# Kernel tuning notes

Hardware: AMD Instinct MI355X
Metric: run time of the kernel (lower is better)

The kernel has to match this reference:

```python
import jax, jax.numpy as jnp
import numpy as np

B, S, D, H, EXPAND = 4, 2048, 256, 4, 4
DH = D // H
EPS = 1e-3  # keras BatchNormalization default epsilon
NEG = -1e9  # keras Softmax masking constant


def setup_inputs() -> dict:
    key = jax.random.key(0)
    ks = jax.random.split(key, 8)
    x = jax.random.normal(ks[0], (B, S, D), dtype=jnp.float32)
    mask = jax.random.randint(ks[1], (B, S), 0, 2) > 0
    mask = mask.at[:, 0].set(True)  # ensure each row has a valid token
    sc = 1.0 / np.sqrt(D)
    return {
        "x": x,
        "mask": mask,
        "bn1_gamma": jnp.ones((D,), jnp.float32),
        "bn1_beta": jnp.zeros((D,), jnp.float32),
        "bn1_mean": jax.random.normal(ks[2], (D,), jnp.float32) * 0.1,
        "bn1_var": jnp.ones((D,), jnp.float32),
        "qkv_w": jax.random.normal(ks[3], (D, 3 * D), jnp.float32) * sc,
        "proj_w": jax.random.normal(ks[4], (D, D), jnp.float32) * sc,
        "bn2_gamma": jnp.ones((D,), jnp.float32),
        "bn2_beta": jnp.zeros((D,), jnp.float32),
        "bn2_mean": jax.random.normal(ks[5], (D,), jnp.float32) * 0.1,
        "bn2_var": jnp.ones((D,), jnp.float32),
        "w1": jax.random.normal(ks[6], (D, EXPAND * D), jnp.float32) * sc,
        "w2": jax.random.normal(ks[7], (EXPAND * D, D), jnp.float32) * (sc / 2.0),
    }


def _bn(x, gamma, beta, mean, var):
    # inference-mode BatchNormalization over the channel axis
    return (x - mean) * jax.lax.rsqrt(var + EPS) * gamma + beta


def reference(x, mask, bn1_gamma, bn1_beta, bn1_mean, bn1_var, qkv_w, proj_w,
              bn2_gamma, bn2_beta, bn2_mean, bn2_var, w1, w2):
    scale = D ** (-0.5)
    # --- attention sub-block ---
    skip = x
    h = _bn(x, bn1_gamma, bn1_beta, bn1_mean, bn1_var)
    qkv = h @ qkv_w                                    # [B,S,3D]
    qkv = qkv.reshape(B, S, H, 3 * DH).transpose(0, 2, 1, 3)  # [B,H,S,3dh]
    q, k, v = qkv[..., :DH], qkv[..., DH:2 * DH], qkv[..., 2 * DH:]
    scores = jnp.einsum('bhqd,bhkd->bhqk', q, k) * scale      # [B,H,S,S]
    scores = scores + jnp.where(mask[:, None, None, :], 0.0, NEG)
    attn = jax.nn.softmax(scores, axis=-1)
    o = jnp.einsum('bhqk,bhkd->bhqd', attn, v)                # [B,H,S,dh]
    o = o.transpose(0, 2, 1, 3).reshape(B, S, D) @ proj_w
    x = o + skip
    # --- FFN sub-block ---
    skip = x
    h = _bn(x, bn2_gamma, bn2_beta, bn2_mean, bn2_var)
    h = jax.nn.swish(h @ w1)                                  # [B,S,4D]
    h = h @ w2
    return h + skip
```

## Files before the change

kernel.cpp:

```cpp
#include <hip/hip_runtime.h>
#include <math.h>

#define S_ 2048
#define D_ 256
#define B_ 4
#define H_ 4

typedef __attribute__((ext_vector_type(8))) short  bh8;
typedef __attribute__((ext_vector_type(4))) float  fx4;
typedef __attribute__((ext_vector_type(4))) unsigned short us4;
typedef __attribute__((ext_vector_type(4))) unsigned int   ux4;

__device__ inline unsigned short bf16r(float f) {
    unsigned int u = __builtin_bit_cast(unsigned int, f);
    return (unsigned short)((u + 0x7FFFu + ((u >> 16) & 1u)) >> 16);
}
__device__ inline unsigned int cvtpk(float a, float b) {
    unsigned int r;
    asm("v_cvt_pk_bf16_f32 %0, %1, %2" : "=v"(r) : "v"(a), "v"(b));
    return r;
}
__device__ inline float vexp2(float x) {
    float r;
    asm volatile("v_exp_f32 %0, %1\n\ts_nop 1" : "=v"(r) : "v"(x));
    return r;
}
__device__ inline void gl_lds16(const unsigned short* g, unsigned short* l) {
    __builtin_amdgcn_global_load_lds(
        (const __attribute__((address_space(1))) unsigned int*)g,
        (__attribute__((address_space(3))) unsigned int*)l, 16, 0, 0);
}
#define DRAIN_BARRIER() asm volatile("s_waitcnt vmcnt(0)\n\ts_barrier" ::: "memory")

__device__ inline size_t fragoff(int m, int k, int K32) {
    return ((size_t)(m >> 4) * K32 + (k >> 5)) * 512
         + (size_t)((((k >> 3) & 3) * 16 + (m & 15)) * 8 + (k & 7));
}

__global__ __launch_bounds__(256) void prep_all_k(
    const float* __restrict__ qkv_w, const float* __restrict__ proj_w,
    const float* __restrict__ w1,    const float* __restrict__ w2,
    unsigned short* __restrict__ qkv_wt, unsigned short* __restrict__ proj_wf,
    unsigned short* __restrict__ w1f,    unsigned short* __restrict__ w2f,
    const float* __restrict__ x,
    const float* __restrict__ g1, const float* __restrict__ b1,
    const float* __restrict__ m1, const float* __restrict__ v1,
    unsigned short* __restrict__ xb,
    const int* __restrict__ mask, float* __restrict__ maskf)
{
    const int bidx = blockIdx.x;
    if (bidx < 768) {
        const float* W; unsigned short* Wt; int K, N, u0; bool frag;
        if (bidx < 192)      { W = qkv_w;  Wt = qkv_wt; K = 256;  N = 768;  u0 = bidx * 256;        frag = false; }
        else if (bidx < 256) { W = proj_w; Wt = proj_wf; K = 256;  N = 256;  u0 = (bidx - 192) * 256; frag = true; }
        else if (bidx < 512) { W = w1;     Wt = w1f;    K = 256;  N = 1024; u0 = (bidx - 256) * 256; frag = true; }
        else                 { W = w2;     Wt = w2f;    K = 1024; N = 256;  u0 = (bidx - 512) * 256; frag = true; }
        const int u = u0 + threadIdx.x;
        const int k4 = u / N, n = u % N;
        us4 tv;
        #pragma unroll
        for (int j = 0; j < 4; ++j) tv[j] = bf16r(W[(size_t)(k4 * 4 + j) * N + n]);
        if (frag) *(us4*)&Wt[fragoff(n, k4 * 4, K >> 5)] = tv;
        else      *(us4*)&Wt[(size_t)n * K + k4 * 4] = tv;
    } else if (bidx < 2816) {
        const int i = (bidx - 768) * 256 + threadIdx.x;
        const int c4 = (i & 63) * 4;
        float4 xv = *(const float4*)&x[(size_t)i * 4];
        float vv[4] = {xv.x, xv.y, xv.z, xv.w};
        us4 tv;
        #pragma unroll
        for (int j = 0; j < 4; ++j) {
            int c = c4 + j;
            float s = g1[c] * rsqrtf(v1[c] + 1e-3f);
            tv[j] = bf16r(vv[j] * s + (b1[c] - m1[c] * s));
        }
        *(us4*)&xb[(size_t)i * 4] = tv;
    } else {
        const int i = (bidx - 2816) * 256 + threadIdx.x;
        maskf[i] = mask[i] ? 0.0f : -1e9f;
    }
}

__global__ __launch_bounds__(256) void gemm_qkv_k(
    const unsigned short* __restrict__ A, const unsigned short* __restrict__ Wt,
    unsigned short* __restrict__ qf_o, unsigned short* __restrict__ kf_o,
    unsigned short* __restrict__ vf_o)
{
    constexpr int BM = 64, MI = 2, LA = 2;
    const int N = 768, K = 256;
    __shared__ unsigned short Asb[2][BM * 64];
    __shared__ unsigned short Bsb[2][128 * 64];

    const int n0 = blockIdx.x * 128, m0 = blockIdx.y * BM;
    const int t = threadIdx.x, w = t >> 6, l = t & 63;
    const int qi = l & 15, g = l >> 4;
    const int wm = w >> 1, wn = w & 1;
    const int lr = l >> 3, lc = (l & 7) * 8;
    (void)N;

    fx4 acc[MI][4];
    #pragma unroll
    for (int mi = 0; mi < MI; ++mi)
        #pragma unroll
        for (int ni = 0; ni < 4; ++ni) acc[mi][ni] = (fx4){0.f, 0.f, 0.f, 0.f};

    const int NT = K / 64;

#define STAGE(P, KT) {                                                        \
    const int kb = (KT) * 64;                                                 \
    _Pragma("unroll")                                                         \
    for (int i = 0; i < LA; ++i) {                                            \
        int r0 = (w * LA + i) * 8;                                            \
        gl_lds16(A + (size_t)(m0 + r0 + lr) * K + kb + lc, &Asb[P][r0 * 64]); \
    }                                                                         \
    _Pragma("unroll")                                                         \
    for (int i = 0; i < 4; ++i) {                                             \
        int r0 = (w * 4 + i) * 8;                                             \
        gl_lds16(Wt + (size_t)(n0 + r0 + lr) * K + kb + lc, &Bsb[P][r0 * 64]);\
    } }

    STAGE(0, 0);
    DRAIN_BARRIER();
    int p = 0;
    for (int kt = 0; kt < NT; ++kt) {
        if (kt + 1 < NT) STAGE(p ^ 1, kt + 1);
        #pragma unroll
        for (int kk = 0; kk < 2; ++kk) {
            bh8 af[MI], bf[4];
            #pragma unroll
            for (int mi = 0; mi < MI; ++mi)
                af[mi] = *(const bh8*)&Asb[p][(wm * (BM / 2) + mi * 16 + qi) * 64
                                             + kk * 32 + g * 8];
            #pragma unroll
            for (int ni = 0; ni < 4; ++ni)
                bf[ni] = *(const bh8*)&Bsb[p][(wn * 64 + ni * 16 + qi) * 64
                                             + kk * 32 + g * 8];
            #pragma unroll
            for (int mi = 0; mi < MI; ++mi)
                #pragma unroll
                for (int ni = 0; ni < 4; ++ni)
                    acc[mi][ni] = __builtin_amdgcn_mfma_f32_16x16x32_bf16(
                        af[mi], bf[ni], acc[mi][ni], 0, 0, 0);
        }
        DRAIN_BARRIER();
        p ^= 1;
    }
#undef STAGE

    const int mbase = m0 + wm * (BM / 2);
    #pragma unroll
    for (int ni = 0; ni < 4; ++ni) {
        const int nf = n0 + wn * 64 + ni * 16;
        const int h = nf / 192, rem = nf % 192;
        const int region = rem / 64;
        const int c = rem % 64 + qi;
        #pragma unroll
        for (int mi = 0; mi < MI; ++mi) {
            #pragma unroll
            for (int r = 0; r < 4; ++r) {
                const int m = mbase + mi * 16 + g * 4 + r;
                const int s = m & 2047;
                const size_t bh = (size_t)((m >> 11) * 4 + h);
                float a = acc[mi][ni][r];
                if (region < 2) {
                    size_t off = (((bh * 128 + (s >> 4)) * 2 + (c >> 5)) * 64
                                  + ((c >> 3) & 3) * 16 + (s & 15)) * 8 + (c & 7);
                    if (region == 0)
                        qf_o[off] = bf16r(a * (0.0625f * 1.44269504f));
                    else
                        kf_o[off] = bf16r(a);
                } else {
                    size_t off = ((((bh * 32 + (s >> 6)) * 4 + (c >> 4)) * 2
                                  + ((s >> 5) & 1)) * 64
                                  + ((s >> 3) & 3) * 16 + (c & 15)) * 8 + (s & 7);
                    vf_o[off] = bf16r(a);
                }
            }
        }
    }
}

__global__ __launch_bounds__(512) void fused_mlp_k(
    const unsigned short* __restrict__ ob,
    const unsigned short* __restrict__ proj_wf,
    const unsigned short* __restrict__ w1f,
    const unsigned short* __restrict__ w2f,
    const float* __restrict__ x,
    const float* __restrict__ g2, const float* __restrict__ b2,
    const float* __restrict__ m2, const float* __restrict__ v2,
    float* __restrict__ out)
{
    __shared__ unsigned short x2nb[8 * 512];
    __shared__ unsigned short h2[32 * 512];

    const int t = threadIdx.x, w = t >> 6, l = t & 63;
    const int qi = l & 15, g = l >> 4;
    const int mt = blockIdx.x;
    const int m0 = mt * 16;

    fx4 acc1[2];
    acc1[0] = (fx4){0.f, 0.f, 0.f, 0.f};
    acc1[1] = (fx4){0.f, 0.f, 0.f, 0.f};
    {
        const unsigned short* Ab = ob + (size_t)mt * 8 * 512 + l * 8;
        const unsigned short* B0 = proj_wf + ((size_t)(w * 2 + 0) * 8) * 512 + l * 8;
        const unsigned short* B1 = proj_wf + ((size_t)(w * 2 + 1) * 8) * 512 + l * 8;
        #pragma unroll
        for (int kt = 0; kt < 8; ++kt) {
            bh8 a  = *(const bh8*)(Ab + (size_t)kt * 512);
            bh8 b0 = *(const bh8*)(B0 + (size_t)kt * 512);
            bh8 b1 = *(const bh8*)(B1 + (size_t)kt * 512);
            acc1[0] = __builtin_amdgcn_mfma_f32_16x16x32_bf16(a, b0, acc1[0], 0, 0, 0);
            acc1[1] = __builtin_amdgcn_mfma_f32_16x16x32_bf16(a, b1, acc1[1], 0, 0, 0);
        }
    }
    float x2res[2][4];
    #pragma unroll
    for (int nt = 0; nt < 2; ++nt) {
        const int n = w * 32 + nt * 16 + qi;
        const float s2 = g2[n] * rsqrtf(v2[n] + 1e-3f);
        const float o2 = b2[n] - m2[n] * s2;
        #pragma unroll
        for (int r = 0; r < 4; ++r) {
            const int m = m0 + g * 4 + r;
            float rv = acc1[nt][r] + x[(size_t)m * 256 + n];
            x2res[nt][r] = rv;
            x2nb[w * 512 + ((nt * 2 + (qi >> 3)) * 16 + g * 4 + r) * 8 + (qi & 7)]
                = bf16r(rv * s2 + o2);
        }
    }
    __syncthreads();

    fx4 acc2[8];
    #pragma unroll
    for (int nt = 0; nt < 8; ++nt) acc2[nt] = (fx4){0.f, 0.f, 0.f, 0.f};
    {
        #pragma unroll
        for (int kt = 0; kt < 8; ++kt) {
            bh8 a = *(const bh8*)&x2nb[kt * 512 + l * 8];
            #pragma unroll
            for (int nt = 0; nt < 8; ++nt) {
                bh8 b = *(const bh8*)(w1f + ((size_t)(w * 8 + nt) * 8 + kt) * 512 + l * 8);
                acc2[nt] = __builtin_amdgcn_mfma_f32_16x16x32_bf16(a, b, acc2[nt], 0, 0, 0);
            }
        }
    }
    __syncthreads();
    #pragma unroll
    for (int nt = 0; nt < 8; ++nt) {
        #pragma unroll
        for (int r = 0; r < 4; ++r) {
            const int n = w * 128 + nt * 16 + qi;
            float a = acc2[nt][r];
            float hv = a / (1.0f + __expf(-a));
            h2[(n >> 5) * 512 + (((n >> 3) & 3) * 16 + g * 4 + r) * 8 + (n & 7)]
                = bf16r(hv);
        }
    }
    __syncthreads();

    fx4 acc3[2];
    acc3[0] = (fx4){0.f, 0.f, 0.f, 0.f};
    acc3[1] = (fx4){0.f, 0.f, 0.f, 0.f};
    {
        const unsigned short* B0 = w2f + ((size_t)(w * 2 + 0) * 32) * 512 + l * 8;
        const unsigned short* B1 = w2f + ((size_t)(w * 2 + 1) * 32) * 512 + l * 8;
        #pragma unroll 4
        for (int kt = 0; kt < 32; ++kt) {
            bh8 a  = *(const bh8*)&h2[kt * 512 + l * 8];
            bh8 b0 = *(const bh8*)(B0 + (size_t)kt * 512);
            bh8 b1 = *(const bh8*)(B1 + (size_t)kt * 512);
            acc3[0] = __builtin_amdgcn_mfma_f32_16x16x32_bf16(a, b0, acc3[0], 0, 0, 0);
            acc3[1] = __builtin_amdgcn_mfma_f32_16x16x32_bf16(a, b1, acc3[1], 0, 0, 0);
        }
    }
    #pragma unroll
    for (int nt = 0; nt < 2; ++nt) {
        #pragma unroll
        for (int r = 0; r < 4; ++r) {
            const int m = m0 + g * 4 + r;
            const int n = w * 32 + nt * 16 + qi;
            out[(size_t)m * 256 + n] = acc3[nt][r] + x2res[nt][r];
        }
    }
}

__global__ __launch_bounds__(256) void attn_mfma_k(
    const unsigned short* __restrict__ qf,
    const unsigned short* __restrict__ kf,
    const unsigned short* __restrict__ vf,
    const float* __restrict__ maskf,
    unsigned short* __restrict__ ob)
{
    __shared__ fx4  Ol[2][64][8];
    __shared__ float Ll[2][64][2];

    const int bid = blockIdx.x;
    const int bh = bid & 15, qt = bid >> 4;
    const int b = bh >> 2, h = bh & 3;
    const int t = threadIdx.x;
    const int w = t >> 6, lane = t & 63;
    const int g = lane >> 4, qi = lane & 15;
    const int qh = w & 1;
    const int khalf = w >> 1;

    bh8 qA0, qA1, qB0, qB1;
    {
        const unsigned short* qp =
            qf + (size_t)(bh * 128 + qt * 4 + qh * 2) * 1024 + lane * 8;
        qA0 = *(const bh8*)(qp);
        qA1 = *(const bh8*)(qp + 512);
        qB0 = *(const bh8*)(qp + 1024);
        qB1 = *(const bh8*)(qp + 1536);
    }

    fx4 oA[4], oB[4];
    #pragma unroll
    for (int dt = 0; dt < 4; ++dt) {
        oA[dt] = (fx4){0.f, 0.f, 0.f, 0.f};
        oB[dt] = (fx4){0.f, 0.f, 0.f, 0.f};
    }
    float lsA = 0.f, lsB = 0.f;

    const unsigned short* kcur = kf + (size_t)bh * 131072 + khalf * 65536 + lane * 8;
    const unsigned short* vcur = vf + (size_t)bh * 131072 + khalf * 65536 + lane * 8;
    const float* mcur = maskf + b * 2048 + khalf * 1024 + g * 4;

    bh8 kfA[4][2], kfB[4][2], afA[4][2], afB[4][2];
    fx4 mvA[4], mvB[4];

#define LOADK(KF, MV) {                                                       \
    KF[0][0] = *(const bh8*)(kcur);        KF[0][1] = *(const bh8*)(kcur + 512);  \
    KF[1][0] = *(const bh8*)(kcur + 1024); KF[1][1] = *(const bh8*)(kcur + 1536); \
    KF[2][0] = *(const bh8*)(kcur + 2048); KF[2][1] = *(const bh8*)(kcur + 2560); \
    KF[3][0] = *(const bh8*)(kcur + 3072); KF[3][1] = *(const bh8*)(kcur + 3584); \
    MV[0] = *(const fx4*)(mcur);      MV[1] = *(const fx4*)(mcur + 16);       \
    MV[2] = *(const fx4*)(mcur + 32); MV[3] = *(const fx4*)(mcur + 48);       \
    kcur += 4096; mcur += 64; }

#define LOADV(AF) {                                                           \
    AF[0][0] = *(const bh8*)(vcur);        AF[0][1] = *(const bh8*)(vcur + 512);  \
    AF[1][0] = *(const bh8*)(vcur + 1024); AF[1][1] = *(const bh8*)(vcur + 1536); \
    AF[2][0] = *(const bh8*)(vcur + 2048); AF[2][1] = *(const bh8*)(vcur + 2560); \
    AF[3][0] = *(const bh8*)(vcur + 3072); AF[3][1] = *(const bh8*)(vcur + 3584); \
    vcur += 4096; }

#define PROCESS(KF, AF, MV) {                                                 \
    fx4 sA[4], sB[4];                                                         \
    _Pragma("unroll")                                                         \
    for (int kt = 0; kt < 4; ++kt) {                                          \
        fx4 zA = MV[kt];                                                      \
        zA = __builtin_amdgcn_mfma_f32_16x16x32_bf16(KF[kt][0], qA0, zA, 0, 0, 0); \
        zA = __builtin_amdgcn_mfma_f32_16x16x32_bf16(KF[kt][1], qA1, zA, 0, 0, 0); \
        sA[kt] = zA;                                                          \
        fx4 zB = MV[kt];                                                      \
        zB = __builtin_amdgcn_mfma_f32_16x16x32_bf16(KF[kt][0], qB0, zB, 0, 0, 0); \
        zB = __builtin_amdgcn_mfma_f32_16x16x32_bf16(KF[kt][1], qB1, zB, 0, 0, 0); \
        sB[kt] = zB;                                                          \
    }                                                                         \
    unsigned int pkA[4][2], pkB[4][2];                                        \
    _Pragma("unroll")                                                         \
    for (int kt = 0; kt < 4; ++kt) {                                          \
        float a0 = vexp2(sA[kt][0]);                                          \
        float a1 = vexp2(sA[kt][1]);                                          \
        float a2 = vexp2(sA[kt][2]);                                          \
        float a3 = vexp2(sA[kt][3]);                                          \
        lsA += (a0 + a1) + (a2 + a3);                                         \
        pkA[kt][0] = cvtpk(a0, a1);                                           \
        pkA[kt][1] = cvtpk(a2, a3);                                           \
        float b0 = vexp2(sB[kt][0]);                                          \
        float b1 = vexp2(sB[kt][1]);                                          \
        float b2 = vexp2(sB[kt][2]);                                          \
        float b3 = vexp2(sB[kt][3]);                                          \
        lsB += (b0 + b1) + (b2 + b3);                                         \
        pkB[kt][0] = cvtpk(b0, b1);                                           \
        pkB[kt][1] = cvtpk(b2, b3);                                           \
    }                                                                         \
    _Pragma("unroll")                                                         \
    for (int c = 0; c < 2; ++c) {                                             \
        unsigned int bwA[4], bwB[4];                                          \
        _Pragma("unroll")                                                     \
        for (int wd = 0; wd < 4; ++wd) {                                      \
            int src = (2 * (g & 1) + (wd >> 1)) * 16 + qi;                    \
            unsigned int vaA = (unsigned int)__shfl((int)pkA[2 * c][wd & 1], src, 64);     \
            unsigned int vbA = (unsigned int)__shfl((int)pkA[2 * c + 1][wd & 1], src, 64); \
            bwA[wd] = (g >= 2) ? vbA : vaA;                                   \
            unsigned int vaB = (unsigned int)__shfl((int)pkB[2 * c][wd & 1], src, 64);     \
            unsigned int vbB = (unsigned int)__shfl((int)pkB[2 * c + 1][wd & 1], src, 64); \
            bwB[wd] = (g >= 2) ? vbB : vaB;                                   \
        }                                                                     \
        bh8 bfA = __builtin_bit_cast(bh8, (ux4){bwA[0], bwA[1], bwA[2], bwA[3]}); \
        bh8 bfB = __builtin_bit_cast(bh8, (ux4){bwB[0], bwB[1], bwB[2], bwB[3]}); \
        _Pragma("unroll")                                                     \
        for (int dt = 0; dt < 4; ++dt) {                                      \
            oA[dt] = __builtin_amdgcn_mfma_f32_16x16x32_bf16(AF[dt][c], bfA, oA[dt], 0, 0, 0); \
            oB[dt] = __builtin_amdgcn_mfma_f32_16x16x32_bf16(AF[dt][c], bfB, oB[dt], 0, 0, 0); \
        }                                                                     \
    } }

    LOADK(kfA, mvA);
    LOADV(afA);
    for (int it = 0; it < 16; it += 2) {
        LOADK(kfB, mvB);
        LOADV(afB);
        PROCESS(kfA, afA, mvA);
        if (it + 2 < 16) {
            LOADK(kfA, mvA);
            LOADV(afA);
        }
        PROCESS(kfB, afB, mvB);
    }
#undef LOADK
#undef LOADV
#undef PROCESS

    const int slot = w & 1;
    if (w >= 2) {
        #pragma unroll
        for (int dt = 0; dt < 4; ++dt) {
            Ol[slot][lane][dt]     = oA[dt];
            Ol[slot][lane][4 + dt] = oB[dt];
        }
        Ll[slot][lane][0] = lsA;
        Ll[slot][lane][1] = lsB;
    }
    __syncthreads();
    if (w < 2) {
        lsA += Ll[slot][lane][0];
        lsB += Ll[slot][lane][1];
        #pragma unroll
        for (int dt = 0; dt < 4; ++dt) {
            fx4 pa = Ol[slot][lane][dt], pb = Ol[slot][lane][4 + dt];
            oA[dt][0] += pa[0]; oA[dt][1] += pa[1]; oA[dt][2] += pa[2]; oA[dt][3] += pa[3];
            oB[dt][0] += pb[0]; oB[dt][1] += pb[1]; oB[dt][2] += pb[2]; oB[dt][3] += pb[3];
        }
        lsA += __shfl_xor(lsA, 16, 64);
        lsA += __shfl_xor(lsA, 32, 64);
        lsB += __shfl_xor(lsB, 16, 64);
        lsB += __shfl_xor(lsB, 32, 64);
        float invA = 1.0f / lsA, invB = 1.0f / lsB;
        const int mA = b * 2048 + qt * 64 + qh * 32 + qi;
        #pragma unroll
        for (int dt = 0; dt < 4; ++dt) {
            us4 ta, tb;
            #pragma unroll
            for (int r = 0; r < 4; ++r) {
                ta[r] = bf16r(oA[dt][r] * invA);
                tb[r] = bf16r(oB[dt][r] * invB);
            }
            const int n0 = h * 64 + dt * 16 + g * 4;
            *(us4*)&ob[fragoff(mA,      n0, 8)] = ta;
            *(us4*)&ob[fragoff(mA + 16, n0, 8)] = tb;
        }
    }
}

extern "C" void kernel_launch(void* const* d_in, const int* in_sizes, int n_in,
                              void* d_out, int out_size, void* d_ws, size_t ws_size,
                              hipStream_t stream) {
    const float* x      = (const float*)d_in[0];
    const int*   mask   = (const int*)  d_in[1];
    const float* bn1_g  = (const float*)d_in[2];
    const float* bn1_b  = (const float*)d_in[3];
    const float* bn1_m  = (const float*)d_in[4];
    const float* bn1_v  = (const float*)d_in[5];
    const float* qkv_w  = (const float*)d_in[6];
    const float* proj_w = (const float*)d_in[7];
    const float* bn2_g  = (const float*)d_in[8];
    const float* bn2_b  = (const float*)d_in[9];
    const float* bn2_m  = (const float*)d_in[10];
    const float* bn2_v  = (const float*)d_in[11];
    const float* w1     = (const float*)d_in[12];
    const float* w2     = (const float*)d_in[13];
    float* out = (float*)d_out;

    char* w8 = (char*)d_ws;
    unsigned short* qkv_wt  = (unsigned short*)(w8 + 0);
    unsigned short* proj_wf = (unsigned short*)(w8 + 393216);
    unsigned short* w1f     = (unsigned short*)(w8 + 524288);
    unsigned short* w2f     = (unsigned short*)(w8 + 1048576);
    float*          maskf   = (float*)         (w8 + 1572864);
    unsigned short* xb      = (unsigned short*)(w8 + 2097152);
    unsigned short* qfrag   = (unsigned short*)(w8 + 18874368);
    unsigned short* kfrag   = (unsigned short*)(w8 + 23068672);
    unsigned short* vfrag   = (unsigned short*)(w8 + 27262976);
    unsigned short* ob      = (unsigned short*)(w8 + 31457280);

    prep_all_k<<<2848, 256, 0, stream>>>(
        qkv_w, proj_w, w1, w2, qkv_wt, proj_wf, w1f, w2f,
        x, bn1_g, bn1_b, bn1_m, bn1_v, xb, mask, maskf);

    gemm_qkv_k<<<dim3(6, 128), 256, 0, stream>>>(
        xb, qkv_wt, qfrag, kfrag, vfrag);

    attn_mfma_k<<<dim3(512), 256, 0, stream>>>(qfrag, kfrag, vfrag, maskf, ob);

    fused_mlp_k<<<dim3(512), 512, 0, stream>>>(
        ob, proj_wf, w1f, w2f, x, bn2_g, bn2_b, bn2_m, bn2_v, out);
}
```

Baseline: 88.93 us.

## Store QKV GEMM operands in MFMA fragment layout and load directly from global

The prep kernel now writes the normalized activations and the QKV weights in MFMA fragment order. The QKV GEMM is rewritten to read each fragment straight from global memory into registers. The old LDS double-buffered tile pipeline and its barriers are gone. Each 512-thread block handles one 16-row M tile across all 768 columns, with 6 N tiles per wave. This removes LDS staging and synchronisation, but it loses LDS reuse: each block rereads the whole weight matrix from cache, and no prefetching overlaps the loads.

Result: slower. 90.80 us (+2.1%).

```diff
diff --git a/kernel.cpp b/kernel.cpp
--- a/kernel.cpp
+++ b/kernel.cpp
@@ -25,12 +25,6 @@
     asm volatile("v_exp_f32 %0, %1\n\ts_nop 1" : "=v"(r) : "v"(x));
     return r;
 }
-__device__ inline void gl_lds16(const unsigned short* g, unsigned short* l) {
-    __builtin_amdgcn_global_load_lds(
-        (const __attribute__((address_space(1))) unsigned int*)g,
-        (__attribute__((address_space(3))) unsigned int*)l, 16, 0, 0);
-}
-#define DRAIN_BARRIER() asm volatile("s_waitcnt vmcnt(0)\n\ts_barrier" ::: "memory")
 
 __device__ inline size_t fragoff(int m, int k, int K32) {
     return ((size_t)(m >> 4) * K32 + (k >> 5)) * 512
@@ -40,141 +34,97 @@
 __global__ __launch_bounds__(256) void prep_all_k(
     const float* __restrict__ qkv_w, const float* __restrict__ proj_w,
     const float* __restrict__ w1,    const float* __restrict__ w2,
-    unsigned short* __restrict__ qkv_wt, unsigned short* __restrict__ proj_wf,
+    unsigned short* __restrict__ qkv_wf, unsigned short* __restrict__ proj_wf,
     unsigned short* __restrict__ w1f,    unsigned short* __restrict__ w2f,
     const float* __restrict__ x,
     const float* __restrict__ g1, const float* __restrict__ b1,
     const float* __restrict__ m1, const float* __restrict__ v1,
-    unsigned short* __restrict__ xb,
+    unsigned short* __restrict__ xbf,
     const int* __restrict__ mask, float* __restrict__ maskf)
 {
     const int bidx = blockIdx.x;
     if (bidx < 768) {
-        const float* W; unsigned short* Wt; int K, N, u0; bool frag;
-        if (bidx < 192)      { W = qkv_w;  Wt = qkv_wt; K = 256;  N = 768;  u0 = bidx * 256;        frag = false; }
-        else if (bidx < 256) { W = proj_w; Wt = proj_wf; K = 256;  N = 256;  u0 = (bidx - 192) * 256; frag = true; }
-        else if (bidx < 512) { W = w1;     Wt = w1f;    K = 256;  N = 1024; u0 = (bidx - 256) * 256; frag = true; }
-        else                 { W = w2;     Wt = w2f;    K = 1024; N = 256;  u0 = (bidx - 512) * 256; frag = true; }
+        const float* W; unsigned short* Wt; int K, N, u0;
+        if (bidx < 192)      { W = qkv_w;  Wt = qkv_wf;  K = 256;  N = 768;  u0 = bidx * 256; }
+        else if (bidx < 256) { W = proj_w; Wt = proj_wf; K = 256;  N = 256;  u0 = (bidx - 192) * 256; }
+        else if (bidx < 512) { W = w1;     Wt = w1f;     K = 256;  N = 1024; u0 = (bidx - 256) * 256; }
+        else                 { W = w2;     Wt = w2f;     K = 1024; N = 256;  u0 = (bidx - 512) * 256; }
         const int u = u0 + threadIdx.x;
         const int k4 = u / N, n = u % N;
         us4 tv;
         #pragma unroll
         for (int j = 0; j < 4; ++j) tv[j] = bf16r(W[(size_t)(k4 * 4 + j) * N + n]);
-        if (frag) *(us4*)&Wt[fragoff(n, k4 * 4, K >> 5)] = tv;
-        else      *(us4*)&Wt[(size_t)n * K + k4 * 4] = tv;
+        *(us4*)&Wt[fragoff(n, k4 * 4, K >> 5)] = tv;
     } else if (bidx < 2816) {
         const int i = (bidx - 768) * 256 + threadIdx.x;
-        const int c4 = (i & 63) * 4;
+        const int m = i >> 6, c0 = (i & 63) * 4;
         float4 xv = *(const float4*)&x[(size_t)i * 4];
         float vv[4] = {xv.x, xv.y, xv.z, xv.w};
         us4 tv;
         #pragma unroll
         for (int j = 0; j < 4; ++j) {
-            int c = c4 + j;
+            int c = c0 + j;
             float s = g1[c] * rsqrtf(v1[c] + 1e-3f);
             tv[j] = bf16r(vv[j] * s + (b1[c] - m1[c] * s));
         }
-        *(us4*)&xb[(size_t)i * 4] = tv;
+        *(us4*)&xbf[fragoff(m, c0, 8)] = tv;
     } else {
         const int i = (bidx - 2816) * 256 + threadIdx.x;
         maskf[i] = mask[i] ? 0.0f : -1e9f;
     }
 }
 
-__global__ __launch_bounds__(256) void gemm_qkv_k(
-    const unsigned short* __restrict__ A, const unsigned short* __restrict__ Wt,
+__global__ __launch_bounds__(512) void gemm_qkv_frag_k(
+    const unsigned short* __restrict__ xbf, const unsigned short* __restrict__ Wf,
     unsigned short* __restrict__ qf_o, unsigned short* __restrict__ kf_o,
     unsigned short* __restrict__ vf_o)
 {
-    constexpr int BM = 64, MI = 2, LA = 2;
-    const int N = 768, K = 256;
-    __shared__ unsigned short Asb[2][BM * 64];
-    __shared__ unsigned short Bsb[2][128 * 64];
-
-    const int n0 = blockIdx.x * 128, m0 = blockIdx.y * BM;
     const int t = threadIdx.x, w = t >> 6, l = t & 63;
     const int qi = l & 15, g = l >> 4;
-    const int wm = w >> 1, wn = w & 1;
-    const int lr = l >> 3, lc = (l & 7) * 8;
-    (void)N;
-
-    fx4 acc[MI][4];
-    #pragma unroll
-    for (int mi = 0; mi < MI; ++mi)
-        #pragma unroll
-        for (int ni = 0; ni < 4; ++ni) acc[mi][ni] = (fx4){0.f, 0.f, 0.f, 0.f};
-
-    const int NT = K / 64;
-
-#define STAGE(P, KT) {                                                        \
-    const int kb = (KT) * 64;                                                 \
-    _Pragma("unroll")                                                         \
-    for (int i = 0; i < LA; ++i) {                                            \
-        int r0 = (w * LA + i) * 8;                                            \
-        gl_lds16(A + (size_t)(m0 + r0 + lr) * K + kb + lc, &Asb[P][r0 * 64]); \
-    }                                                                         \
-    _Pragma("unroll")                                                         \
-    for (int i = 0; i < 4; ++i) {                                             \
-        int r0 = (w * 4 + i) * 8;                                             \
-        gl_lds16(Wt + (size_t)(n0 + r0 + lr) * K + kb + lc, &Bsb[P][r0 * 64]);\
-    } }
-
-    STAGE(0, 0);
-    DRAIN_BARRIER();
-    int p = 0;
-    for (int kt = 0; kt < NT; ++kt) {
-        if (kt + 1 < NT) STAGE(p ^ 1, kt + 1);
-        #pragma unroll
-        for (int kk = 0; kk < 2; ++kk) {
-            bh8 af[MI], bf[4];
-            #pragma unroll
-            for (int mi = 0; mi < MI; ++mi)
-                af[mi] = *(const bh8*)&Asb[p][(wm * (BM / 2) + mi * 16 + qi) * 64
-                                             + kk * 32 + g * 8];
-            #pragma unroll
-            for (int ni = 0; ni < 4; ++ni)
-                bf[ni] = *(const bh8*)&Bsb[p][(wn * 64 + ni * 16 + qi) * 64
-                                             + kk * 32 + g * 8];
-            #pragma unroll
-            for (int mi = 0; mi < MI; ++mi)
-                #pragma unroll
-                for (int ni = 0; ni < 4; ++ni)
-                    acc[mi][ni] = __builtin_amdgcn_mfma_f32_16x16x32_bf16(
-                        af[mi], bf[ni], acc[mi][ni], 0, 0, 0);
-        }
-        DRAIN_BARRIER();
-        p ^= 1;
-    }
-#undef STAGE
-
-    const int mbase = m0 + wm * (BM / 2);
-    #pragma unroll
-    for (int ni = 0; ni < 4; ++ni) {
-        const int nf = n0 + wn * 64 + ni * 16;
+    const int mt = blockIdx.x;
+    const int nt0 = w * 6;
+
+    fx4 acc[6];
+    #pragma unroll
+    for (int j = 0; j < 6; ++j) acc[j] = (fx4){0.f, 0.f, 0.f, 0.f};
+
+    const unsigned short* Ab = xbf + (size_t)mt * 8 * 512 + l * 8;
+    const unsigned short* Bb = Wf + (size_t)nt0 * 8 * 512 + l * 8;
+
+    #pragma unroll
+    for (int kt = 0; kt < 8; ++kt) {
+        bh8 a = *(const bh8*)(Ab + (size_t)kt * 512);
+        #pragma unroll
+        for (int j = 0; j < 6; ++j) {
+            bh8 b = *(const bh8*)(Bb + ((size_t)j * 8 + kt) * 512);
+            acc[j] = __builtin_amdgcn_mfma_f32_16x16x32_bf16(a, b, acc[j], 0, 0, 0);
+        }
+    }
+
+    #pragma unroll
+    for (int j = 0; j < 6; ++j) {
+        const int nf = (nt0 + j) * 16;
         const int h = nf / 192, rem = nf % 192;
         const int region = rem / 64;
         const int c = rem % 64 + qi;
         #pragma unroll
-        for (int mi = 0; mi < MI; ++mi) {
-            #pragma unroll
-            for (int r = 0; r < 4; ++r) {
-                const int m = mbase + mi * 16 + g * 4 + r;
-                const int s = m & 2047;
-                const size_t bh = (size_t)((m >> 11) * 4 + h);
-                float a = acc[mi][ni][r];
-                if (region < 2) {
-                    size_t off = (((bh * 128 + (s >> 4)) * 2 + (c >> 5)) * 64
-                                  + ((c >> 3) & 3) * 16 + (s & 15)) * 8 + (c & 7);
-                    if (region == 0)
-                        qf_o[off] = bf16r(a * (0.0625f * 1.44269504f));
-                    else
-                        kf_o[off] = bf16r(a);
-                } else {
-                    size_t off = ((((bh * 32 + (s >> 6)) * 4 + (c >> 4)) * 2
-                                  + ((s >> 5) & 1)) * 64
-                                  + ((s >> 3) & 3) * 16 + (c & 15)) * 8 + (s & 7);
-                    vf_o[off] = bf16r(a);
-                }
+        for (int r = 0; r < 4; ++r) {
+            const int m = mt * 16 + g * 4 + r;
+            const int s = m & 2047;
+            const size_t bh = (size_t)((m >> 11) * 4 + h);
+            float a = acc[j][r];
+            if (region < 2) {
+                size_t off = (((bh * 128 + (s >> 4)) * 2 + (c >> 5)) * 64
+                              + ((c >> 3) & 3) * 16 + (s & 15)) * 8 + (c & 7);
+                if (region == 0)
+                    qf_o[off] = bf16r(a * (0.0625f * 1.44269504f));
+                else
+                    kf_o[off] = bf16r(a);
+            } else {
+                size_t off = ((((bh * 32 + (s >> 6)) * 4 + (c >> 4)) * 2
+                              + ((s >> 5) & 1)) * 64
+                              + ((s >> 3) & 3) * 16 + (c & 15)) * 8 + (s & 7);
+                vf_o[off] = bf16r(a);
             }
         }
     }
@@ -475,23 +425,23 @@
     float* out = (float*)d_out;
 
     char* w8 = (char*)d_ws;
-    unsigned short* qkv_wt  = (unsigned short*)(w8 + 0);
+    unsigned short* qkv_wf  = (unsigned short*)(w8 + 0);
     unsigned short* proj_wf = (unsigned short*)(w8 + 393216);
     unsigned short* w1f     = (unsigned short*)(w8 + 524288);
     unsigned short* w2f     = (unsigned short*)(w8 + 1048576);
     float*          maskf   = (float*)         (w8 + 1572864);
-    unsigned short* xb      = (unsigned short*)(w8 + 2097152);
+    unsigned short* xbf     = (unsigned short*)(w8 + 2097152);
     unsigned short* qfrag   = (unsigned short*)(w8 + 18874368);
     unsigned short* kfrag   = (unsigned short*)(w8 + 23068672);
     unsigned short* vfrag   = (unsigned short*)(w8 + 27262976);
     unsigned short* ob      = (unsigned short*)(w8 + 31457280);
 
     prep_all_k<<<2848, 256, 0, stream>>>(
-        qkv_w, proj_w, w1, w2, qkv_wt, proj_wf, w1f, w2f,
-        x, bn1_g, bn1_b, bn1_m, bn1_v, xb, mask, maskf);
-
-    gemm_qkv_k<<<dim3(6, 128), 256, 0, stream>>>(
-        xb, qkv_wt, qfrag, kfrag, vfrag);
+        qkv_w, proj_w, w1, w2, qkv_wf, proj_wf, w1f, w2f,
+        x, bn1_g, bn1_b, bn1_m, bn1_v, xbf, mask, maskf);
+
+    gemm_qkv_frag_k<<<dim3(512), 512, 0, stream>>>(
+        xbf, qkv_wf, qfrag, kfrag, vfrag);
 
     attn_mfma_k<<<dim3(512), 256, 0, stream>>>(qfrag, kfrag, vfrag, maskf, ob);
 
```
